# Optimization experiments

Hardware: AMD Instinct MI355X
Metric: run time of the kernel (lower is better)

The kernel has to match this reference:

```python
import jax, jax.numpy as jnp
import numpy as np

UINT8_MAX = 255.0
SUBPIXEL_EPS = 1e-6
MAX_SUBPIXEL_MAGNITUDE = 1.0


def spiral_pattern_np(sz):
    """Spiral traversal pattern, identical to the torch reference."""
    pattern = np.zeros((2 * sz + 1, 2 * sz + 1), dtype=np.float32)
    radius = sz
    n = 0
    for dy in range(radius + 1):
        for direction in range(4):
            limit = 1 if (direction == 0 and dy == 0) else dy
            for dx in range(-dy, limit):
                if direction == 0:
                    wx, wy = radius + dx, radius + dy
                elif direction == 1:
                    wx, wy = radius + dy, radius - dx
                elif direction == 2:
                    wx, wy = radius - dx, radius - dy
                else:
                    wx, wy = radius - dy, radius + dx
                n += 1
                pattern[wy, wx] = n
    return pattern


def binomial(img):
    # separable [1 2 1]/4 blur, replicate padding; img: [B,1,H,W]
    p = jnp.pad(img, ((0, 0), (0, 0), (1, 1), (0, 0)), mode='edge')
    v = (p[:, :, :-2, :] + 2.0 * img + p[:, :, 2:, :]) / 4.0
    p = jnp.pad(v, ((0, 0), (0, 0), (0, 0), (1, 1)), mode='edge')
    return (p[:, :, :, :-2] + 2.0 * v + p[:, :, :, 2:]) / 4.0


def gradient(f):
    p = jnp.pad(f, ((0, 0), (0, 0), (1, 1), (1, 1)), mode='edge')
    gy = (p[:, :, 2:, 1:-1] - p[:, :, :-2, 1:-1]) / 2.0
    gx = (p[:, :, 1:-1, 2:] - p[:, :, 1:-1, :-2]) / 2.0
    return gy, gx


def blocks(img, T):
    # [B,1,H,W] -> non-overlapping T x T templates flattened: [B, H//T, W//T, T*T]
    B = img.shape[0]
    H, W = img.shape[2], img.shape[3]
    x = img.reshape(B, H // T, T, W // T, T)
    return x.transpose(0, 1, 3, 2, 4).reshape(B, H // T, W // T, T * T)


def calculate_flow(img_cur, img_prev, T, R):
    cur = binomial(img_cur)
    prev = binomial(img_prev)
    # emulate cast-to-uint8 quantization of the reference pipeline
    q = lambda x: jnp.clip(jnp.round(x * UINT8_MAX), 0.0, UINT8_MAX)
    cur_q, prev_q = q(cur), q(prev)

    templates = blocks(cur_q, T)                       # [B,Hb,Wb,T2]
    B, Hb, Wb, T2 = templates.shape
    H, W = img_cur.shape[2], img_cur.shape[3]

    # candidate shifted blocks (search windows): [B,Hb,Wb,C,T2], C=(2R+1)^2
    pad_prev = jnp.pad(prev_q, ((0, 0), (0, 0), (R, R), (R, R)), mode='edge')
    cands = [blocks(pad_prev[:, :, R + dy:R + dy + H, R + dx:R + dx + W], T)
             for dy in range(-R, R + 1) for dx in range(-R, R + 1)]
    windows = jnp.stack(cands, axis=3)

    # SAD cost volume: [B,Hb,Wb,C]
    cost = jnp.sum(jnp.abs(windows - templates[:, :, :, None, :]), axis=-1)

    # spiral-tie-break argmin (equivalent to ArgMinCentered mode='spiral':
    # among min-cost candidates, pick the one earliest in the spiral order)
    spir = jnp.asarray(spiral_pattern_np(R).reshape(-1), dtype=jnp.float32)
    min_c = jnp.min(cost, axis=-1, keepdims=True)
    tie = jnp.where(cost == min_c, spir, jnp.inf)
    idx = jnp.argmin(tie, axis=-1)                     # [B,Hb,Wb]

    rng = jnp.arange(-R, R + 1, dtype=jnp.float32)
    jj, ii = jnp.meshgrid(rng, rng, indexing='ij')
    vec_lut = -1.0 * jnp.stack([jj, ii], axis=-1).reshape(-1, 2)
    vec = vec_lut[idx]                                 # [B,Hb,Wb,2] = [-dy,-dx]

    # 3x3 median filter (replicate pad) on the vector field [B,2,Hb,Wb]
    v = vec.transpose(0, 3, 1, 2)
    vp = jnp.pad(v, ((0, 0), (0, 0), (1, 1), (1, 1)), mode='edge')
    patches = jnp.stack([vp[:, :, i:i + Hb, j:j + Wb]
                         for i in range(3) for j in range(3)], axis=2)
    v_med = jnp.median(patches, axis=2)                # [B,2,Hb,Wb]

    # gather the matched block at the (rounded) median vector
    med_i = jnp.clip(jnp.round(v_med), -R, R).astype(jnp.int32)
    off_y, off_x = -med_i[:, 0], -med_i[:, 1]          # vec stores negated offsets
    cand_idx = (off_y + R) * (2 * R + 1) + (off_x + R) # [B,Hb,Wb]
    idxe = jnp.broadcast_to(cand_idx[..., None, None], (B, Hb, Wb, 1, T2))
    matched = jnp.take_along_axis(windows, idxe, axis=3)[:, :, :, 0, :]

    # Lucas-Kanade subpixel refinement (border-ring weighted)
    tmpl = templates / UINT8_MAX
    mat = matched / UINT8_MAX
    gy_img, gx_img = gradient(cur)
    gy = blocks(gy_img, T)
    gx = blocks(gx_img, T)
    pred = jnp.pad(jnp.zeros((T - 2, T - 2), jnp.float32), ((1, 1), (1, 1)),
                   constant_values=1.0).reshape(-1)
    rs = lambda x: jnp.sum(x, axis=-1)                 # [B,Hb,Wb]
    a = rs(gx * gx * pred)
    b = rs(gx * gy * pred)
    d = rs(gy * gy * pred)
    diff = mat - tmpl
    p = rs(diff * gx * pred)
    qv = rs(diff * gy * pred)
    det = a * d - b * b
    safe_det = jnp.where(det <= SUBPIXEL_EPS, 1.0, det)
    sub_u = (d * p - b * qv) / safe_det
    sub_v = (a * qv - b * p) / safe_det
    sub = jnp.stack([sub_v, sub_u], axis=-1)           # [B,Hb,Wb,2] (y,x)
    invalid = (det[..., None] <= SUBPIXEL_EPS) | (jnp.abs(sub) >= MAX_SUBPIXEL_MAGNITUDE)
    sub = jnp.where(invalid, 0.0, sub)

    flow = v_med + sub.transpose(0, 3, 1, 2)           # [B,2,Hb,Wb]
    return flow.astype(jnp.float32)


def setup_inputs() -> dict:
    key = jax.random.key(0)
    k1, k2 = jax.random.split(key)
    img_cur = jax.random.uniform(k1, (1, 1, 544, 960), dtype=jnp.float32)
    img_prev = jax.random.uniform(k2, (1, 1, 544, 960), dtype=jnp.float32)
    return {"img_cur": img_cur, "img_prev": img_prev,
            "template_sz": 8, "search_range": 4}


def reference(img_cur, img_prev, template_sz, search_range):
    return calculate_flow(img_cur, img_prev, template_sz, search_range)
```

## Files before the change

### kernel.cpp

```cpp
#include <hip/hip_runtime.h>

#define H  544
#define W  960
#define T  8
#define R  4
#define HB (H / T)
#define WB (W / T)
#define NB (HB * WB)
#define NC 81
#define WIN 16
#define SPB 3
#define GRID (NB / (4 * SPB))
#define TAG 0x51C0u

__device__ __forceinline__ int iclamp(int v, int lo, int hi) {
    return v < lo ? lo : (v > hi ? hi : v);
}

struct SpiralTab { int v[NC]; };

__host__ __device__ constexpr SpiralTab make_spiral() {
    SpiralTab t{};
    int n = 0;
    for (int dy = 0; dy <= R; ++dy) {
        for (int dir = 0; dir < 4; ++dir) {
            int limit = (dir == 0 && dy == 0) ? 1 : dy;
            for (int dx = -dy; dx < limit; ++dx) {
                int wx, wy;
                if (dir == 0)      { wx = R + dx; wy = R + dy; }
                else if (dir == 1) { wx = R + dy; wy = R - dx; }
                else if (dir == 2) { wx = R - dx; wy = R - dy; }
                else               { wx = R - dy; wy = R + dx; }
                t.v[n] = (wy << 4) | wx;
                ++n;
            }
        }
    }
    return t;
}

static __constant__ SpiralTab SPIR = make_spiral();

__device__ __forceinline__ unsigned int sadu8(unsigned int a, unsigned int b, unsigned int acc) {
#if __has_builtin(__builtin_amdgcn_sad_u8)
    return __builtin_amdgcn_sad_u8(a, b, acc);
#else
    unsigned int d;
    asm("v_sad_u8 %0, %1, %2, %3" : "=v"(d) : "v"(a), "v"(b), "v"(acc));
    return d;
#endif
}

__device__ __forceinline__ unsigned int alignb(unsigned int hi, unsigned int lo, unsigned int sh) {
#if __has_builtin(__builtin_amdgcn_alignbyte)
    return __builtin_amdgcn_alignbyte(hi, lo, sh);
#else
    unsigned int d;
    asm("v_alignbyte_b32 %0, %1, %2, %3" : "=v"(d) : "v"(hi), "v"(lo), "v"(sh));
    return d;
#endif
}

#define VERT(a, b, c) (__fmul_rn(__fadd_rn(__fadd_rn((a), __fmul_rn(2.0f, (b))), (c)), 0.25f))
#define QU(h) ((unsigned int)fminf(fmaxf(rintf(__fmul_rn((h), 255.0f)), 0.0f), 255.0f))

__device__ __forceinline__ void msort(float& a, float& b) {
    float mn = fminf(a, b), mx = fmaxf(a, b);
    a = mn; b = mx;
}

__device__ __forceinline__ float median9(float p[9]) {
    msort(p[1], p[2]); msort(p[4], p[5]); msort(p[7], p[8]);
    msort(p[0], p[1]); msort(p[3], p[4]); msort(p[6], p[7]);
    msort(p[1], p[2]); msort(p[4], p[5]); msort(p[7], p[8]);
    msort(p[0], p[3]); msort(p[5], p[8]); msort(p[4], p[7]);
    msort(p[3], p[6]); msort(p[1], p[4]); msort(p[2], p[5]);
    msort(p[4], p[7]); msort(p[4], p[2]); msort(p[6], p[4]);
    msort(p[4], p[2]);
    return p[4];
}

__device__ __forceinline__ unsigned int wait_word(unsigned int* p) {
    unsigned int v = __hip_atomic_load(p, __ATOMIC_RELAXED, __HIP_MEMORY_SCOPE_AGENT);
    while ((v >> 16) != TAG) {
        __builtin_amdgcn_s_sleep(1);
        v = __hip_atomic_load(p, __ATOMIC_RELAXED, __HIP_MEMORY_SCOPE_AGENT);
    }
    return v;
}

__global__ void __launch_bounds__(256, 4)
k_fused(const float* __restrict__ cur, const float* __restrict__ prev,
        unsigned int* __restrict__ vecw, float* __restrict__ out) {
    __shared__ float vb[4][WIN][20];
    __shared__ float vc[4][10][12];
    __shared__ uint4 regionS[4][SPB][WIN];
    __shared__ uint2 tmplS[4][SPB][T];
    __shared__ float gyS[4][SPB][28];
    __shared__ float gxS[4][SPB][28];

    const int wv   = (int)(threadIdx.x >> 6);
    const int lane = (int)(threadIdx.x & 63);
    const int waveId = (int)blockIdx.x * 4 + wv;

    int rty, rtx;
    {
        int k = (lane < 28) ? lane : 0;
        if (k < 8)       { rty = 0;      rtx = k;      }
        else if (k < 16) { rty = T - 1;  rtx = k - 8;  }
        else if (k < 22) { rty = k - 15; rtx = 0;      }
        else             { rty = k - 21; rtx = T - 1;  }
    }

    for (int s = 0; s < SPB; ++s) {
        int bidx = waveId * SPB + s;
        int byi = bidx / WB, bxi = bidx % WB;
        int by0 = byi * T, bx0 = bxi * T;

        for (int e = lane; e < WIN * 18; e += 64) {
            int ry = e / 18, cx = e - ry * 18;
            int gy = iclamp(by0 - R + ry, 0, H - 1);
            int gx = iclamp(bx0 - 5 + cx, 0, W - 1);
            int ym = iclamp(gy - 1, 0, H - 1) * W;
            int yp = iclamp(gy + 1, 0, H - 1) * W;
            vb[wv][ry][cx] = VERT(prev[ym + gx], prev[gy * W + gx], prev[yp + gx]);
        }
        for (int e = lane; e < 120; e += 64) {
            int ry = e / 12, cx = e - ry * 12;
            int gy = iclamp(by0 - 1 + ry, 0, H - 1);
            int gx = iclamp(bx0 - 2 + cx, 0, W - 1);
            int ym = iclamp(gy - 1, 0, H - 1) * W;
            int yp = iclamp(gy + 1, 0, H - 1) * W;
            vc[wv][ry][cx] = VERT(cur[ym + gx], cur[gy * W + gx], cur[yp + gx]);
        }
        __syncthreads();

        {
            unsigned char* regB = (unsigned char*)&regionS[wv][s][0];
            int base = bx0 - 5;
            for (int e = lane; e < WIN * WIN; e += 64) {
                int ry = e >> 4, rx = e & 15;
                int gxp = iclamp(bx0 - R + rx, 0, W - 1);
                int xm = (gxp > 0) ? gxp - 1 : 0;
                int xp = (gxp < W - 1) ? gxp + 1 : W - 1;
                float h = VERT(vb[wv][ry][xm - base], vb[wv][ry][gxp - base], vb[wv][ry][xp - base]);
                regB[ry * 16 + rx] = (unsigned char)QU(h);
            }
        }
        {
            int ty = lane >> 3, tx = lane & 7;
            float hT = VERT(vc[wv][ty + 1][tx + 1], vc[wv][ty + 1][tx + 2], vc[wv][ty + 1][tx + 3]);
            ((unsigned char*)&tmplS[wv][s][0])[ty * 8 + tx] = (unsigned char)QU(hT);
        }
        if (lane < 28) {
            int y = by0 + rty, x = bx0 + rtx;
            int rp = iclamp(y + 1, 0, H - 1) - by0;
            int rm = iclamp(y - 1, 0, H - 1) - by0;
            int cp = iclamp(x + 1, 0, W - 1) - bx0;
            int cm = iclamp(x - 1, 0, W - 1) - bx0;
            float hyp = VERT(vc[wv][rp + 1][rtx + 1], vc[wv][rp + 1][rtx + 2], vc[wv][rp + 1][rtx + 3]);
            float hym = VERT(vc[wv][rm + 1][rtx + 1], vc[wv][rm + 1][rtx + 2], vc[wv][rm + 1][rtx + 3]);
            float hxp = VERT(vc[wv][rty + 1][cp + 1], vc[wv][rty + 1][cp + 2], vc[wv][rty + 1][cp + 3]);
            float hxm = VERT(vc[wv][rty + 1][cm + 1], vc[wv][rty + 1][cm + 2], vc[wv][rty + 1][cm + 3]);
            gyS[wv][s][lane] = (hyp - hym) * 0.5f;
            gxS[wv][s][lane] = (hxp - hxm) * 0.5f;
        }
        __syncthreads();

        unsigned int t0[T], t1[T];
#pragma unroll
        for (int ty = 0; ty < T; ++ty) {
            uint2 tt = tmplS[wv][s][ty];
            t0[ty] = tt.x;
            t1[ty] = tt.y;
        }
        int cell0 = SPIR.v[lane];
        int dy0 = cell0 >> 4, dx0 = cell0 & 15;
        bool v1 = (lane + 64) < NC;
        int cell1 = SPIR.v[v1 ? (lane + 64) : 0];
        int dy1 = cell1 >> 4, dx1 = cell1 & 15;

        unsigned int sad0 = 0, sad1 = 0;
        int q0 = dx0 >> 2; unsigned int r0 = (unsigned int)(dx0 & 3);
        int q1 = dx1 >> 2; unsigned int r1 = (unsigned int)(dx1 & 3);
#pragma unroll
        for (int ty = 0; ty < T; ++ty) {
            {
                uint4 row = regionS[wv][s][ty + dy0];
                unsigned int w0 = (q0 == 0) ? row.x : ((q0 == 1) ? row.y : row.z);
                unsigned int w1 = (q0 == 0) ? row.y : ((q0 == 1) ? row.z : row.w);
                unsigned int w2 = (q0 == 0) ? row.z : row.w;
                sad0 = sadu8(alignb(w1, w0, r0), t0[ty], sad0);
                sad0 = sadu8(alignb(w2, w1, r0), t1[ty], sad0);
            }
            if (v1) {
                uint4 row = regionS[wv][s][ty + dy1];
                unsigned int w0 = (q1 == 0) ? row.x : ((q1 == 1) ? row.y : row.z);
                unsigned int w1 = (q1 == 0) ? row.y : ((q1 == 1) ? row.z : row.w);
                unsigned int w2 = (q1 == 0) ? row.z : row.w;
                sad1 = sadu8(alignb(w1, w0, r1), t0[ty], sad1);
                sad1 = sadu8(alignb(w2, w1, r1), t1[ty], sad1);
            }
        }
        int key = (int)((sad0 << 7) | (unsigned int)lane);
        if (v1) {
            int k1 = (int)((sad1 << 7) | (unsigned int)(lane + 64));
            key = min(key, k1);
        }
#pragma unroll
        for (int off = 32; off > 0; off >>= 1)
            key = min(key, __shfl_xor(key, off));
        if (lane == 0) {
            int rank = key & 127;
            int cell = SPIR.v[rank];
            int vy = -((cell >> 4) - R);
            int vx = -((cell & 15) - R);
            unsigned int word = (TAG << 16) | ((unsigned int)(vy + 8) << 8) | (unsigned int)(vx + 8);
            __hip_atomic_store(&vecw[bidx], word, __ATOMIC_RELAXED, __HIP_MEMORY_SCOPE_AGENT);
        }
    }
    __syncthreads();

    for (int s = 0; s < SPB; ++s) {
        int bidx = waveId * SPB + s;
        int byi = bidx / WB, bxi = bidx % WB;
        int by0 = byi * T, bx0 = bxi * T;

        float py[9], px[9];
#pragma unroll
        for (int i = 0; i < 3; ++i)
#pragma unroll
            for (int j = 0; j < 3; ++j) {
                int nb = iclamp(byi + i - 1, 0, HB - 1) * WB + iclamp(bxi + j - 1, 0, WB - 1);
                unsigned int wd = wait_word(&vecw[nb]);
                py[i * 3 + j] = (float)((int)((wd >> 8) & 255u) - 8);
                px[i * 3 + j] = (float)((int)(wd & 255u) - 8);
            }
        float vmy = median9(py);
        float vmx = median9(px);

        int med_y = iclamp((int)rintf(vmy), -R, R);
        int med_x = iclamp((int)rintf(vmx), -R, R);
        int off_y = -med_y, off_x = -med_x;

        bool act = lane < 28;
        float a = 0.f, b = 0.f, d = 0.f, p = 0.f, q = 0.f;
        if (act) {
            unsigned int tb = ((const unsigned char*)&tmplS[wv][s][0])[rty * 8 + rtx];
            float tmplv = (float)tb / 255.0f;
            int ridx = rty + off_y + R + R;
            ridx = rty + off_y + 4;
            int cidx = rtx + off_x + 4;
            uint4 row = regionS[wv][s][ridx];
            unsigned int wsel = (cidx >> 2) == 0 ? row.x : ((cidx >> 2) == 1 ? row.y : ((cidx >> 2) == 2 ? row.z : row.w));
            unsigned int mb = (wsel >> ((cidx & 3) * 8)) & 255u;
            float matv = (float)mb / 255.0f;
            float gyv = gyS[wv][s][lane];
            float gxv = gxS[wv][s][lane];
            float diff = matv - tmplv;
            a = gxv * gxv;
            b = gxv * gyv;
            d = gyv * gyv;
            p = diff * gxv;
            q = diff * gyv;
        }
#pragma unroll
        for (int off = 16; off > 0; off >>= 1) {
            a += __shfl_xor(a, off);
            b += __shfl_xor(b, off);
            d += __shfl_xor(d, off);
            p += __shfl_xor(p, off);
            q += __shfl_xor(q, off);
        }
        if (lane == 0) {
            float det  = a * d - b * b;
            float safe = (det <= 1e-6f) ? 1.0f : det;
            float su = (d * p - b * q) / safe;
            float sv = (a * q - b * p) / safe;
            bool inval = (det <= 1e-6f);
            float sy = (inval || fabsf(sv) >= 1.0f) ? 0.0f : sv;
            float sx = (inval || fabsf(su) >= 1.0f) ? 0.0f : su;
            out[bidx]      = vmy + sy;
            out[NB + bidx] = vmx + sx;
        }
    }
}

extern "C" void kernel_launch(void* const* d_in, const int* in_sizes, int n_in,
                              void* d_out, int out_size, void* d_ws, size_t ws_size,
                              hipStream_t stream) {
    const float* cur  = (const float*)d_in[0];
    const float* prev = (const float*)d_in[1];
    float* out = (float*)d_out;
    unsigned int* vecw = (unsigned int*)d_ws;

    k_fused<<<GRID, 256, 0, stream>>>(cur, prev, vecw, out);
}
```

Before: 82.04 us.

## Assign one image block per wave and drop the per-wave block loop

The kernel now assigns exactly one 8x8 block to each wave instead of three. This triples the grid size and raises the launch-bounds occupancy hint from 4 to 8 blocks per CU. Gradients stay in registers instead of being staged through shared memory, and the per-block shared arrays shrink. The aim is more parallelism and shorter serial chains per wave. The risk is that the cross-block spin-wait on neighbour motion vectors needs all 2040 workgroups to be co-resident, or it may stall.

```diff
diff --git a/kernel.cpp b/kernel.cpp
--- a/kernel.cpp
+++ b/kernel.cpp
@@ -9,8 +9,7 @@
 #define NB (HB * WB)
 #define NC 81
 #define WIN 16
-#define SPB 3
-#define GRID (NB / (4 * SPB))
+#define GRID (NB / 4)
 #define TAG 0x51C0u
 
 __device__ __forceinline__ int iclamp(int v, int lo, int hi) {
@@ -89,19 +88,19 @@
     return v;
 }
 
-__global__ void __launch_bounds__(256, 4)
+__global__ void __launch_bounds__(256, 8)
 k_fused(const float* __restrict__ cur, const float* __restrict__ prev,
         unsigned int* __restrict__ vecw, float* __restrict__ out) {
     __shared__ float vb[4][WIN][20];
     __shared__ float vc[4][10][12];
-    __shared__ uint4 regionS[4][SPB][WIN];
-    __shared__ uint2 tmplS[4][SPB][T];
-    __shared__ float gyS[4][SPB][28];
-    __shared__ float gxS[4][SPB][28];
+    __shared__ uint4 regionS[4][WIN];
+    __shared__ uint2 tmplS[4][T];
 
     const int wv   = (int)(threadIdx.x >> 6);
     const int lane = (int)(threadIdx.x & 63);
-    const int waveId = (int)blockIdx.x * 4 + wv;
+    const int bidx = (int)blockIdx.x * 4 + wv;
+    const int byi = bidx / WB, bxi = bidx % WB;
+    const int by0 = byi * T, bx0 = bxi * T;
 
     int rty, rtx;
     {
@@ -112,177 +111,158 @@
         else             { rty = k - 21; rtx = T - 1;  }
     }
 
-    for (int s = 0; s < SPB; ++s) {
-        int bidx = waveId * SPB + s;
-        int byi = bidx / WB, bxi = bidx % WB;
-        int by0 = byi * T, bx0 = bxi * T;
-
-        for (int e = lane; e < WIN * 18; e += 64) {
-            int ry = e / 18, cx = e - ry * 18;
-            int gy = iclamp(by0 - R + ry, 0, H - 1);
-            int gx = iclamp(bx0 - 5 + cx, 0, W - 1);
-            int ym = iclamp(gy - 1, 0, H - 1) * W;
-            int yp = iclamp(gy + 1, 0, H - 1) * W;
-            vb[wv][ry][cx] = VERT(prev[ym + gx], prev[gy * W + gx], prev[yp + gx]);
-        }
-        for (int e = lane; e < 120; e += 64) {
-            int ry = e / 12, cx = e - ry * 12;
-            int gy = iclamp(by0 - 1 + ry, 0, H - 1);
-            int gx = iclamp(bx0 - 2 + cx, 0, W - 1);
-            int ym = iclamp(gy - 1, 0, H - 1) * W;
-            int yp = iclamp(gy + 1, 0, H - 1) * W;
-            vc[wv][ry][cx] = VERT(cur[ym + gx], cur[gy * W + gx], cur[yp + gx]);
-        }
-        __syncthreads();
-
+    for (int e = lane; e < WIN * 18; e += 64) {
+        int ry = e / 18, cx = e - ry * 18;
+        int gy = iclamp(by0 - R + ry, 0, H - 1);
+        int gx = iclamp(bx0 - 5 + cx, 0, W - 1);
+        int ym = iclamp(gy - 1, 0, H - 1) * W;
+        int yp = iclamp(gy + 1, 0, H - 1) * W;
+        vb[wv][ry][cx] = VERT(prev[ym + gx], prev[gy * W + gx], prev[yp + gx]);
+    }
+    for (int e = lane; e < 120; e += 64) {
+        int ry = e / 12, cx = e - ry * 12;
+        int gy = iclamp(by0 - 1 + ry, 0, H - 1);
+        int gx = iclamp(bx0 - 2 + cx, 0, W - 1);
+        int ym = iclamp(gy - 1, 0, H - 1) * W;
+        int yp = iclamp(gy + 1, 0, H - 1) * W;
+        vc[wv][ry][cx] = VERT(cur[ym + gx], cur[gy * W + gx], cur[yp + gx]);
+    }
+    __syncthreads();
+
+    {
+        unsigned char* regB = (unsigned char*)&regionS[wv][0];
+        int base = bx0 - 5;
+        for (int e = lane; e < WIN * WIN; e += 64) {
+            int ry = e >> 4, rx = e & 15;
+            int gxp = iclamp(bx0 - R + rx, 0, W - 1);
+            int xm = (gxp > 0) ? gxp - 1 : 0;
+            int xp = (gxp < W - 1) ? gxp + 1 : W - 1;
+            float h = VERT(vb[wv][ry][xm - base], vb[wv][ry][gxp - base], vb[wv][ry][xp - base]);
+            regB[ry * 16 + rx] = (unsigned char)QU(h);
+        }
+    }
+    {
+        int ty = lane >> 3, tx = lane & 7;
+        float hT = VERT(vc[wv][ty + 1][tx + 1], vc[wv][ty + 1][tx + 2], vc[wv][ty + 1][tx + 3]);
+        ((unsigned char*)&tmplS[wv][0])[ty * 8 + tx] = (unsigned char)QU(hT);
+    }
+    float gyv = 0.0f, gxv = 0.0f;
+    if (lane < 28) {
+        int y = by0 + rty, x = bx0 + rtx;
+        int rp = iclamp(y + 1, 0, H - 1) - by0;
+        int rm = iclamp(y - 1, 0, H - 1) - by0;
+        int cp = iclamp(x + 1, 0, W - 1) - bx0;
+        int cm = iclamp(x - 1, 0, W - 1) - bx0;
+        float hyp = VERT(vc[wv][rp + 1][rtx + 1], vc[wv][rp + 1][rtx + 2], vc[wv][rp + 1][rtx + 3]);
+        float hym = VERT(vc[wv][rm + 1][rtx + 1], vc[wv][rm + 1][rtx + 2], vc[wv][rm + 1][rtx + 3]);
+        float hxp = VERT(vc[wv][rty + 1][cp + 1], vc[wv][rty + 1][cp + 2], vc[wv][rty + 1][cp + 3]);
+        float hxm = VERT(vc[wv][rty + 1][cm + 1], vc[wv][rty + 1][cm + 2], vc[wv][rty + 1][cm + 3]);
+        gyv = (hyp - hym) * 0.5f;
+        gxv = (hxp - hxm) * 0.5f;
+    }
+    __syncthreads();
+
+    int cell0 = SPIR.v[lane];
+    int dy0 = cell0 >> 4, dx0 = cell0 & 15;
+    bool v1 = (lane + 64) < NC;
+    int cell1 = SPIR.v[v1 ? (lane + 64) : 0];
+    int dy1 = cell1 >> 4, dx1 = cell1 & 15;
+
+    unsigned int sad0 = 0, sad1 = 0;
+    int q0 = dx0 >> 2; unsigned int r0 = (unsigned int)(dx0 & 3);
+    int q1 = dx1 >> 2; unsigned int r1 = (unsigned int)(dx1 & 3);
+#pragma unroll
+    for (int ty = 0; ty < T; ++ty) {
+        uint2 tt = tmplS[wv][ty];
         {
-            unsigned char* regB = (unsigned char*)&regionS[wv][s][0];
-            int base = bx0 - 5;
-            for (int e = lane; e < WIN * WIN; e += 64) {
-                int ry = e >> 4, rx = e & 15;
-                int gxp = iclamp(bx0 - R + rx, 0, W - 1);
-                int xm = (gxp > 0) ? gxp - 1 : 0;
-                int xp = (gxp < W - 1) ? gxp + 1 : W - 1;
-                float h = VERT(vb[wv][ry][xm - base], vb[wv][ry][gxp - base], vb[wv][ry][xp - base]);
-                regB[ry * 16 + rx] = (unsigned char)QU(h);
-            }
-        }
-        {
-            int ty = lane >> 3, tx = lane & 7;
-            float hT = VERT(vc[wv][ty + 1][tx + 1], vc[wv][ty + 1][tx + 2], vc[wv][ty + 1][tx + 3]);
-            ((unsigned char*)&tmplS[wv][s][0])[ty * 8 + tx] = (unsigned char)QU(hT);
-        }
-        if (lane < 28) {
-            int y = by0 + rty, x = bx0 + rtx;
-            int rp = iclamp(y + 1, 0, H - 1) - by0;
-            int rm = iclamp(y - 1, 0, H - 1) - by0;
-            int cp = iclamp(x + 1, 0, W - 1) - bx0;
-            int cm = iclamp(x - 1, 0, W - 1) - bx0;
-            float hyp = VERT(vc[wv][rp + 1][rtx + 1], vc[wv][rp + 1][rtx + 2], vc[wv][rp + 1][rtx + 3]);
-            float hym = VERT(vc[wv][rm + 1][rtx + 1], vc[wv][rm + 1][rtx + 2], vc[wv][rm + 1][rtx + 3]);
-            float hxp = VERT(vc[wv][rty + 1][cp + 1], vc[wv][rty + 1][cp + 2], vc[wv][rty + 1][cp + 3]);
-            float hxm = VERT(vc[wv][rty + 1][cm + 1], vc[wv][rty + 1][cm + 2], vc[wv][rty + 1][cm + 3]);
-            gyS[wv][s][lane] = (hyp - hym) * 0.5f;
-            gxS[wv][s][lane] = (hxp - hxm) * 0.5f;
-        }
-        __syncthreads();
-
-        unsigned int t0[T], t1[T];
-#pragma unroll
-        for (int ty = 0; ty < T; ++ty) {
-            uint2 tt = tmplS[wv][s][ty];
-            t0[ty] = tt.x;
-            t1[ty] = tt.y;
-        }
-        int cell0 = SPIR.v[lane];
-        int dy0 = cell0 >> 4, dx0 = cell0 & 15;
-        bool v1 = (lane + 64) < NC;
-        int cell1 = SPIR.v[v1 ? (lane + 64) : 0];
-        int dy1 = cell1 >> 4, dx1 = cell1 & 15;
-
-        unsigned int sad0 = 0, sad1 = 0;
-        int q0 = dx0 >> 2; unsigned int r0 = (unsigned int)(dx0 & 3);
-        int q1 = dx1 >> 2; unsigned int r1 = (unsigned int)(dx1 & 3);
-#pragma unroll
-        for (int ty = 0; ty < T; ++ty) {
-            {
-                uint4 row = regionS[wv][s][ty + dy0];
-                unsigned int w0 = (q0 == 0) ? row.x : ((q0 == 1) ? row.y : row.z);
-                unsigned int w1 = (q0 == 0) ? row.y : ((q0 == 1) ? row.z : row.w);
-                unsigned int w2 = (q0 == 0) ? row.z : row.w;
-                sad0 = sadu8(alignb(w1, w0, r0), t0[ty], sad0);
-                sad0 = sadu8(alignb(w2, w1, r0), t1[ty], sad0);
-            }
-            if (v1) {
-                uint4 row = regionS[wv][s][ty + dy1];
-                unsigned int w0 = (q1 == 0) ? row.x : ((q1 == 1) ? row.y : row.z);
-                unsigned int w1 = (q1 == 0) ? row.y : ((q1 == 1) ? row.z : row.w);
-                unsigned int w2 = (q1 == 0) ? row.z : row.w;
-                sad1 = sadu8(alignb(w1, w0, r1), t0[ty], sad1);
-                sad1 = sadu8(alignb(w2, w1, r1), t1[ty], sad1);
-            }
-        }
-        int key = (int)((sad0 << 7) | (unsigned int)lane);
+            uint4 row = regionS[wv][ty + dy0];
+            unsigned int w0 = (q0 == 0) ? row.x : ((q0 == 1) ? row.y : row.z);
+            unsigned int w1 = (q0 == 0) ? row.y : ((q0 == 1) ? row.z : row.w);
+            unsigned int w2 = (q0 == 0) ? row.z : row.w;
+            sad0 = sadu8(alignb(w1, w0, r0), tt.x, sad0);
+            sad0 = sadu8(alignb(w2, w1, r0), tt.y, sad0);
+        }
         if (v1) {
-            int k1 = (int)((sad1 << 7) | (unsigned int)(lane + 64));
-            key = min(key, k1);
-        }
-#pragma unroll
-        for (int off = 32; off > 0; off >>= 1)
-            key = min(key, __shfl_xor(key, off));
-        if (lane == 0) {
-            int rank = key & 127;
-            int cell = SPIR.v[rank];
-            int vy = -((cell >> 4) - R);
-            int vx = -((cell & 15) - R);
-            unsigned int word = (TAG << 16) | ((unsigned int)(vy + 8) << 8) | (unsigned int)(vx + 8);
-            __hip_atomic_store(&vecw[bidx], word, __ATOMIC_RELAXED, __HIP_MEMORY_SCOPE_AGENT);
-        }
-    }
-    __syncthreads();
-
-    for (int s = 0; s < SPB; ++s) {
-        int bidx = waveId * SPB + s;
-        int byi = bidx / WB, bxi = bidx % WB;
-        int by0 = byi * T, bx0 = bxi * T;
-
-        float py[9], px[9];
-#pragma unroll
-        for (int i = 0; i < 3; ++i)
-#pragma unroll
-            for (int j = 0; j < 3; ++j) {
-                int nb = iclamp(byi + i - 1, 0, HB - 1) * WB + iclamp(bxi + j - 1, 0, WB - 1);
-                unsigned int wd = wait_word(&vecw[nb]);
-                py[i * 3 + j] = (float)((int)((wd >> 8) & 255u) - 8);
-                px[i * 3 + j] = (float)((int)(wd & 255u) - 8);
-            }
-        float vmy = median9(py);
-        float vmx = median9(px);
-
-        int med_y = iclamp((int)rintf(vmy), -R, R);
-        int med_x = iclamp((int)rintf(vmx), -R, R);
-        int off_y = -med_y, off_x = -med_x;
-
-        bool act = lane < 28;
-        float a = 0.f, b = 0.f, d = 0.f, p = 0.f, q = 0.f;
-        if (act) {
-            unsigned int tb = ((const unsigned char*)&tmplS[wv][s][0])[rty * 8 + rtx];
-            float tmplv = (float)tb / 255.0f;
-            int ridx = rty + off_y + R + R;
-            ridx = rty + off_y + 4;
-            int cidx = rtx + off_x + 4;
-            uint4 row = regionS[wv][s][ridx];
-            unsigned int wsel = (cidx >> 2) == 0 ? row.x : ((cidx >> 2) == 1 ? row.y : ((cidx >> 2) == 2 ? row.z : row.w));
-            unsigned int mb = (wsel >> ((cidx & 3) * 8)) & 255u;
-            float matv = (float)mb / 255.0f;
-            float gyv = gyS[wv][s][lane];
-            float gxv = gxS[wv][s][lane];
-            float diff = matv - tmplv;
-            a = gxv * gxv;
-            b = gxv * gyv;
-            d = gyv * gyv;
-            p = diff * gxv;
-            q = diff * gyv;
-        }
-#pragma unroll
-        for (int off = 16; off > 0; off >>= 1) {
-            a += __shfl_xor(a, off);
-            b += __shfl_xor(b, off);
-            d += __shfl_xor(d, off);
-            p += __shfl_xor(p, off);
-            q += __shfl_xor(q, off);
-        }
-        if (lane == 0) {
-            float det  = a * d - b * b;
-            float safe = (det <= 1e-6f) ? 1.0f : det;
-            float su = (d * p - b * q) / safe;
-            float sv = (a * q - b * p) / safe;
-            bool inval = (det <= 1e-6f);
-            float sy = (inval || fabsf(sv) >= 1.0f) ? 0.0f : sv;
-            float sx = (inval || fabsf(su) >= 1.0f) ? 0.0f : su;
-            out[bidx]      = vmy + sy;
-            out[NB + bidx] = vmx + sx;
-        }
+            uint4 row = regionS[wv][ty + dy1];
+            unsigned int w0 = (q1 == 0) ? row.x : ((q1 == 1) ? row.y : row.z);
+            unsigned int w1 = (q1 == 0) ? row.y : ((q1 == 1) ? row.z : row.w);
+            unsigned int w2 = (q1 == 0) ? row.z : row.w;
+            sad1 = sadu8(alignb(w1, w0, r1), tt.x, sad1);
+            sad1 = sadu8(alignb(w2, w1, r1), tt.y, sad1);
+        }
+    }
+    int key = (int)((sad0 << 7) | (unsigned int)lane);
+    if (v1) {
+        int k1 = (int)((sad1 << 7) | (unsigned int)(lane + 64));
+        key = min(key, k1);
+    }
+#pragma unroll
+    for (int off = 32; off > 0; off >>= 1)
+        key = min(key, __shfl_xor(key, off));
+    if (lane == 0) {
+        int rank = key & 127;
+        int cell = SPIR.v[rank];
+        int vy = -((cell >> 4) - R);
+        int vx = -((cell & 15) - R);
+        unsigned int word = (TAG << 16) | ((unsigned int)(vy + 8) << 8) | (unsigned int)(vx + 8);
+        __hip_atomic_store(&vecw[bidx], word, __ATOMIC_RELAXED, __HIP_MEMORY_SCOPE_AGENT);
+    }
+
+    float py[9], px[9];
+#pragma unroll
+    for (int i = 0; i < 3; ++i)
+#pragma unroll
+        for (int j = 0; j < 3; ++j) {
+            int nb = iclamp(byi + i - 1, 0, HB - 1) * WB + iclamp(bxi + j - 1, 0, WB - 1);
+            unsigned int wd = wait_word(&vecw[nb]);
+            py[i * 3 + j] = (float)((int)((wd >> 8) & 255u) - 8);
+            px[i * 3 + j] = (float)((int)(wd & 255u) - 8);
+        }
+    float vmy = median9(py);
+    float vmx = median9(px);
+
+    int med_y = iclamp((int)rintf(vmy), -R, R);
+    int med_x = iclamp((int)rintf(vmx), -R, R);
+    int off_y = -med_y, off_x = -med_x;
+
+    bool act = lane < 28;
+    float a = 0.f, b = 0.f, d = 0.f, p = 0.f, q = 0.f;
+    if (act) {
+        unsigned int tb = ((const unsigned char*)&tmplS[wv][0])[rty * 8 + rtx];
+        float tmplv = (float)tb / 255.0f;
+        int ridx = rty + off_y + 4;
+        int cidx = rtx + off_x + 4;
+        uint4 row = regionS[wv][ridx];
+        unsigned int wsel = (cidx >> 2) == 0 ? row.x
+                          : ((cidx >> 2) == 1 ? row.y
+                          : ((cidx >> 2) == 2 ? row.z : row.w));
+        unsigned int mb = (wsel >> ((cidx & 3) * 8)) & 255u;
+        float matv = (float)mb / 255.0f;
+        float diff = matv - tmplv;
+        a = gxv * gxv;
+        b = gxv * gyv;
+        d = gyv * gyv;
+        p = diff * gxv;
+        q = diff * gyv;
+    }
+#pragma unroll
+    for (int off = 16; off > 0; off >>= 1) {
+        a += __shfl_xor(a, off);
+        b += __shfl_xor(b, off);
+        d += __shfl_xor(d, off);
+        p += __shfl_xor(p, off);
+        q += __shfl_xor(q, off);
+    }
+    if (lane == 0) {
+        float det  = a * d - b * b;
+        float safe = (det <= 1e-6f) ? 1.0f : det;
+        float su = (d * p - b * q) / safe;
+        float sv = (a * q - b * p) / safe;
+        bool inval = (det <= 1e-6f);
+        float sy = (inval || fabsf(sv) >= 1.0f) ? 0.0f : sv;
+        float sx = (inval || fabsf(su) >= 1.0f) ? 0.0f : su;
+        out[bidx]      = vmy + sy;
+        out[NB + bidx] = vmx + sx;
     }
 }
 
```

Result: no change. 82.20 us (+0.2%).
